# Kernel tuning notes

Hardware: AMD Instinct MI355X
Metric: run time of the kernel (lower is better)

Reference implementation:

```python
import jax, jax.numpy as jnp
import numpy as np

N = 100000
IN_DIM = 256
HID = 64
HEADS = 2
OUT_DIM = 64
E = 1600000
NEG_SLOPE = 0.2


def gat_conv(x, edge_index, W, att_src, att_dst, bias):
    # PyG GATConv with heads=HEADS, concat=True, add_self_loops=True.
    # x: [N, IN_DIM]; edge_index: [2, E] (row0=src, row1=dst)
    loops = jnp.arange(N, dtype=edge_index.dtype)
    src = jnp.concatenate([edge_index[0], loops])  # [E+N]
    dst = jnp.concatenate([edge_index[1], loops])  # [E+N]
    h = (x @ W).reshape(N, HEADS, HID)             # [N, H, C]
    a_src = jnp.einsum('nhc,hc->nh', h, att_src)   # [N, H]
    a_dst = jnp.einsum('nhc,hc->nh', h, att_dst)   # [N, H]
    e = jax.nn.leaky_relu(a_src[src] + a_dst[dst], NEG_SLOPE)  # [E+N, H]
    # segment softmax over incoming edges of each dst node
    m = jax.ops.segment_max(e, dst, num_segments=N)            # [N, H]
    p = jnp.exp(e - m[dst])
    denom = jax.ops.segment_sum(p, dst, num_segments=N)        # [N, H]
    alpha = p / denom[dst]                                     # [E+N, H]
    msg = h[src] * alpha[:, :, None]                           # [E+N, H, C]
    out = jax.ops.segment_sum(msg, dst, num_segments=N)        # [N, H, C]
    return out.reshape(N, HEADS * HID) + bias


def setup_inputs() -> dict:
    key = jax.random.key(0)
    ks = jax.random.split(key, 12)
    s_in = 1.0 / np.sqrt(IN_DIM)
    s_h = 1.0 / np.sqrt(HID)
    s_fc = 1.0 / np.sqrt(HEADS * HID * 2)
    return {
        'x': jax.random.normal(ks[0], (N, IN_DIM), jnp.float32),
        'edge_index_connected': jax.random.randint(ks[1], (2, E), 0, N, jnp.int32),
        'edge_index_liked': jax.random.randint(ks[2], (2, E), 0, N, jnp.int32),
        'W1': jax.random.normal(ks[3], (IN_DIM, HEADS * HID), jnp.float32) * s_in,
        'att_src1': jax.random.normal(ks[4], (HEADS, HID), jnp.float32) * s_h,
        'att_dst1': jax.random.normal(ks[5], (HEADS, HID), jnp.float32) * s_h,
        'b1': jnp.zeros((HEADS * HID,), jnp.float32),
        'W2': jax.random.normal(ks[6], (IN_DIM, HEADS * HID), jnp.float32) * s_in,
        'att_src2': jax.random.normal(ks[7], (HEADS, HID), jnp.float32) * s_h,
        'att_dst2': jax.random.normal(ks[8], (HEADS, HID), jnp.float32) * s_h,
        'b2': jnp.zeros((HEADS * HID,), jnp.float32),
        'fc_W': jax.random.normal(ks[9], (HEADS * HID * 2, OUT_DIM), jnp.float32) * s_fc,
        'fc_b': jnp.zeros((OUT_DIM,), jnp.float32),
    }


def reference(x, edge_index_connected, edge_index_liked, W1, att_src1, att_dst1, b1,
              W2, att_src2, att_dst2, b2, fc_W, fc_b):
    xc = jax.nn.relu(gat_conv(x, edge_index_connected, W1, att_src1, att_dst1, b1))
    xl = jax.nn.relu(gat_conv(x, edge_index_liked, W2, att_src2, att_dst2, b2))
    x_comb = jnp.concatenate([xc, xl], axis=1)  # [N, 4*HID]
    return x_comb @ fc_W + fc_b
```

## Files before the change

### kernel.cpp

```cpp
#include <hip/hip_runtime.h>
#include <hip/hip_fp16.h>
#include <math.h>

#define NN 100000
#define IN_DIM 256
#define HCH 128
#define OUT_DIM 64
#define EE 1600000
#define NEG_SLOPE 0.2f

#define NB 1024
#define NPB 98
#define CAP 2048

#define GEMM_BLOCKS 1563
#define CONV_BLOCKS 320
#define BUCKET_PER_LAYER 512
#define SORT_BLOCKS (2 * NB)

typedef _Float16 half8v __attribute__((ext_vector_type(8)));
typedef _Float16 half4v __attribute__((ext_vector_type(4)));
typedef __fp16 fp16x2 __attribute__((ext_vector_type(2)));
typedef float float4v __attribute__((ext_vector_type(4)));
typedef unsigned int u32;

union H2U { u32 u; fp16x2 h; };

__device__ __forceinline__ float lrelu(float v) { return v > 0.f ? v : NEG_SLOPE * v; }

__global__ __launch_bounds__(256, 8) void prep_kernel(
    const float* __restrict__ W0, const float* __restrict__ W1,
    const float* __restrict__ fcW,
    _Float16* __restrict__ wt, _Float16* __restrict__ fcw2,
    const int* __restrict__ ei0, const int* __restrict__ ei1,
    int* __restrict__ gcursor, int* __restrict__ bstore)
{
    __shared__ int hist[NB];
    __shared__ int base[NB];
    const int tid = threadIdx.x;

    if (blockIdx.x < CONV_BLOCKS) {
        int i = blockIdx.x * 256 + tid;
        if (i < 2 * IN_DIM * HCH) {
            int l = i >> 15, rem = i & 32767;
            int c = rem >> 8, k = rem & 255;
            const float* W = l ? W1 : W0;
            wt[i] = (_Float16)W[(size_t)k * HCH + c];
            return;
        }
        int j = i - 2 * IN_DIM * HCH;
        if (j < 256 * OUT_DIM) {
            int c = j >> 8, k = j & 255;
            fcw2[j] = (_Float16)fcW[(size_t)k * OUT_DIM + c];
        }
        return;
    }

    const int bb = blockIdx.x - CONV_BLOCKS;
    const int lay = bb >> 9;
    const int idx = bb & 511;
    const int* src = lay ? ei1 : ei0;
    const int* dst = src + EE;
    int* gcur = gcursor + lay * NB;
    int* bst = bstore + (size_t)lay * NB * CAP;

    const int per = (EE + BUCKET_PER_LAYER - 1) / BUCKET_PER_LAYER;
    const int e0 = idx * per;
    const int e1 = min(EE, e0 + per);
    for (int i = tid; i < NB; i += 256) hist[i] = 0;
    __syncthreads();
    for (int i = e0 + tid; i < e1; i += 256)
        atomicAdd(&hist[dst[i] / NPB], 1);
    __syncthreads();
    for (int b = tid; b < NB; b += 256) {
        int c = hist[b];
        base[b] = c ? atomicAdd(&gcur[b], c) : 0;
        hist[b] = 0;
    }
    __syncthreads();
    for (int i = e0 + tid; i < e1; i += 256) {
        int d = dst[i];
        int s = src[i];
        int b = d / NPB;
        int pos = base[b] + atomicAdd(&hist[b], 1);
        if (pos >= 0 && pos < CAP) bst[b * CAP + pos] = (s << 7) | (d - b * NPB);
    }
}

__global__ __launch_bounds__(256, 3) void mid_kernel(
    const float* __restrict__ x, const _Float16* __restrict__ wt,
    const float* __restrict__ attS0, const float* __restrict__ attD0,
    const float* __restrict__ attS1, const float* __restrict__ attD1,
    _Float16* __restrict__ h16, float* __restrict__ a_s, float* __restrict__ a_d,
    const int* __restrict__ gcursor, int* __restrict__ bstore,
    int* __restrict__ gstart, int* __restrict__ gend, int n)
{
    __shared__ __align__(16) _Float16 smem[64 * 72 + 256 * 72];
    __shared__ float attv[4][128];
    const int tid = threadIdx.x;

    const long long TS = SORT_BLOCKS;
    const long long TB = GEMM_BLOCKS + SORT_BLOCKS;
    const int k = blockIdx.x;
    const int slo = (int)(((long long)k * TS) / TB);
    const int shi = (int)(((long long)(k + 1) * TS) / TB);

    if (shi > slo) {
        int* raw = (int*)smem;
        int* sorted = raw + CAP;
        int* curs = sorted + CAP;
        int* scanbuf = curs + 128;
        const int sb = slo;
        const int lay = sb >> 10;
        const int b = sb & (NB - 1);
        const int* gcur = gcursor + lay * NB;
        int* bst = bstore + (size_t)lay * NB * CAP;
        int* gs = gstart + (size_t)lay * NN;
        int* ge = gend + (size_t)lay * NN;

        const int node0 = b * NPB;
        const int nnode = min(NPB, n - node0);
        if (nnode <= 0) return;
        int cnt = gcur[b];
        cnt = cnt < 0 ? 0 : (cnt > CAP ? CAP : cnt);

        for (int i = tid; i < cnt; i += 256) raw[i] = bst[b * CAP + i];
        if (tid < 128) curs[tid] = 0;
        __syncthreads();
        for (int i = tid; i < cnt; i += 256) atomicAdd(&curs[raw[i] & 127], 1);
        __syncthreads();
        if (tid < 128) scanbuf[tid] = curs[tid];
        __syncthreads();
        for (int off = 1; off < 128; off <<= 1) {
            int v = 0;
            if (tid < 128) { v = scanbuf[tid]; if (tid >= off) v += scanbuf[tid - off]; }
            __syncthreads();
            if (tid < 128) scanbuf[tid] = v;
            __syncthreads();
        }
        if (tid < 128) {
            int ex = tid ? scanbuf[tid - 1] : 0;
            curs[tid] = ex;
            if (tid < nnode) {
                gs[node0 + tid] = b * CAP + ex;
                ge[node0 + tid] = b * CAP + scanbuf[tid];
            }
        }
        __syncthreads();
        for (int i = tid; i < cnt; i += 256) {
            int item = raw[i];
            int pos = atomicAdd(&curs[item & 127], 1);
            if (pos >= 0 && pos < CAP) sorted[pos] = item >> 7;
        }
        __syncthreads();
        for (int i = tid; i < cnt; i += 256) bst[b * CAP + i] = sorted[i];
        return;
    }

    _Float16 (*As)[72] = (_Float16(*)[72])smem;
    _Float16 (*Bs)[72] = (_Float16(*)[72])(smem + 64 * 72);
    const int gb = k - slo;
    const int lane = tid & 63, wave = tid >> 6;
    const int wm = wave & 1, wn = wave >> 1;
    const int q = lane >> 4, r16 = lane & 15;
    const int row0 = gb * 64;

    if (tid < 128) {
        attv[0][tid] = attS0[tid]; attv[1][tid] = attD0[tid];
        attv[2][tid] = attS1[tid]; attv[3][tid] = attD1[tid];
    }

    float4v acc[2][8];
#pragma unroll
    for (int i = 0; i < 2; ++i)
#pragma unroll
        for (int j = 0; j < 8; ++j) acc[i][j] = (float4v){0.f, 0.f, 0.f, 0.f};

    const int ar = tid >> 2, aq = tid & 3;
    const bool rok = (row0 + ar) < n;
    for (int kt = 0; kt < IN_DIM; kt += 64) {
        const float* xp = x + (size_t)(row0 + ar) * IN_DIM + kt + aq * 16;
#pragma unroll
        for (int i = 0; i < 4; ++i) {
            float4 v = rok ? *(const float4*)(xp + i * 4) : make_float4(0.f, 0.f, 0.f, 0.f);
            half4v hv = { (_Float16)v.x, (_Float16)v.y, (_Float16)v.z, (_Float16)v.w };
            *(half4v*)&As[ar][aq * 16 + i * 4] = hv;
        }
        const _Float16* wp = wt + (size_t)tid * IN_DIM + kt;
#pragma unroll
        for (int i = 0; i < 8; ++i)
            *(half8v*)&Bs[tid][i * 8] = *(const half8v*)(wp + i * 8);
        __syncthreads();
#pragma unroll
        for (int s = 0; s < 2; ++s) {
            half8v af[2], bf[8];
#pragma unroll
            for (int t = 0; t < 2; ++t)
                af[t] = *(half8v*)&As[wm * 32 + t * 16 + r16][s * 32 + q * 8];
#pragma unroll
            for (int t = 0; t < 8; ++t)
                bf[t] = *(half8v*)&Bs[wn * 128 + t * 16 + r16][s * 32 + q * 8];
#pragma unroll
            for (int mt = 0; mt < 2; ++mt)
#pragma unroll
                for (int nt = 0; nt < 8; ++nt)
                    acc[mt][nt] = __builtin_amdgcn_mfma_f32_16x16x32_f16(
                        af[mt], bf[nt], acc[mt][nt], 0, 0, 0);
        }
        __syncthreads();
    }
    _Float16 (*eb)[264] = (_Float16(*)[264])smem;
#pragma unroll
    for (int mt = 0; mt < 2; ++mt) {
        const int er = wm * 32 + mt * 16 + q * 4;
#pragma unroll
        for (int reg = 0; reg < 4; ++reg)
#pragma unroll
            for (int nt = 0; nt < 8; ++nt)
                eb[er + reg][wn * 128 + nt * 16 + r16] = (_Float16)acc[mt][nt][reg];
    }
    __syncthreads();
    const int r = tid >> 2, qq = tid & 3;
    const int grow = row0 + r;
    if (grow < n) {
        const int l2 = qq >> 1;
        const int hh = qq & 1;
        const float* avS = &attv[l2 * 2 + 0][hh * 64];
        const float* avD = &attv[l2 * 2 + 1][hh * 64];
        _Float16* hout = h16 + (size_t)l2 * NN * HCH + (size_t)grow * HCH + hh * 64;
        float ds = 0.f, dd = 0.f;
#pragma unroll
        for (int i = 0; i < 8; ++i) {
            half8v v = *(half8v*)&eb[r][qq * 64 + i * 8];
            *(half8v*)(hout + i * 8) = v;
#pragma unroll
            for (int j = 0; j < 8; ++j) {
                float f = (float)v[j];
                ds = fmaf(f, avS[i * 8 + j], ds);
                dd = fmaf(f, avD[i * 8 + j], dd);
            }
        }
        a_s[(size_t)l2 * 2 * NN + 2 * grow + hh] = ds;
        a_d[(size_t)l2 * 2 * NN + 2 * grow + hh] = dd;
    }
}

__global__ __launch_bounds__(256) void agg_kernel(
    const _Float16* __restrict__ h16, const float2* __restrict__ a_s,
    const float2* __restrict__ a_d, const int* __restrict__ gstart,
    const int* __restrict__ gend, const int* __restrict__ bstore,
    const float* __restrict__ bias0, const float* __restrict__ bias1,
    _Float16* __restrict__ xc16, int n)
{
    __shared__ __align__(16) uint2 sh[4][64];
    const int lay = blockIdx.y;
    const _Float16* hL = h16 + (size_t)lay * NN * HCH;
    const float2* asL = a_s + (size_t)lay * NN;
    const float2* adL = a_d + (size_t)lay * NN;
    const int* gsL = gstart + (size_t)lay * NN;
    const int* geL = gend + (size_t)lay * NN;
    const int* ssort = bstore + (size_t)lay * NB * CAP;
    const float* bias = lay ? bias1 : bias0;

    const int wid = threadIdx.x >> 6, lane = threadIdx.x & 63;
    const int g = lane >> 4;
    const int i = lane & 15;
    const int hh = i >> 3;
    const u32 psel = hh ? 0x07060302u : 0x05040100u;
    const fp16x2 one2 = { (__fp16)1.f, (__fp16)1.f };

    const int node = blockIdx.x * 16 + wid * 4 + g;
    const bool valid = node < n;
    const int nn = valid ? node : 0;

    float bv[8];
#pragma unroll
    for (int j = 0; j < 8; ++j) bv[j] = bias[i * 8 + j];

    int start = gsL[nn], end = geL[nn];
    start = start < 0 ? 0 : (start > NB * CAP ? NB * CAP : start);
    end = end < start ? start : (end > NB * CAP ? NB * CAP : end);
    const int cnt = end - start;
    const float2 ad = adL[nn];
    const float2 asn = asL[nn];

    float acc[8] = {0.f, 0.f, 0.f, 0.f, 0.f, 0.f, 0.f, 0.f};
    float den = 0.f;
    uint2* slots = &sh[wid][g * 16];

    for (int base = 0; base < cnt; base += 16) {
        const int idx = start + base + i;
        float p0 = 0.f, p1 = 0.f;
        int s = 0;
        if (idx < end) {
            s = ssort[idx];
            if ((unsigned)s >= (unsigned)n) s = 0;
            float2 a = asL[s];
            p0 = __expf(lrelu(a.x + ad.x));
            p1 = __expf(lrelu(a.y + ad.y));
        }
        H2U pk; pk.h = __builtin_amdgcn_cvt_pkrtz(p0, p1);
        slots[i] = make_uint2((u32)s, pk.u);
        __builtin_amdgcn_wave_barrier();
        const int c2 = min(16, cnt - base);
        for (int t = 0; t < c2; t += 2) {
            const uint4 rec = *(const uint4*)&slots[t];
            H2U pph; pph.u = __builtin_amdgcn_perm(rec.w, rec.y, psel);
            const half8v hv0 = *(const half8v*)(hL + ((rec.x << 7) | (u32)(i << 3)));
            const half8v hv1 = *(const half8v*)(hL + ((rec.z << 7) | (u32)(i << 3)));
            const u32* ap = (const u32*)&hv0;
            const u32* bp = (const u32*)&hv1;
#pragma unroll
            for (int d2 = 0; d2 < 4; ++d2) {
                H2U pe, po;
                pe.u = __builtin_amdgcn_perm(bp[d2], ap[d2], 0x05040100u);
                po.u = __builtin_amdgcn_perm(bp[d2], ap[d2], 0x07060302u);
                acc[2 * d2]     = __builtin_amdgcn_fdot2(pe.h, pph.h, acc[2 * d2], false);
                acc[2 * d2 + 1] = __builtin_amdgcn_fdot2(po.h, pph.h, acc[2 * d2 + 1], false);
            }
            den = __builtin_amdgcn_fdot2(pph.h, one2, den, false);
        }
        __builtin_amdgcn_wave_barrier();
    }
    {
        const float ps0 = __expf(lrelu(asn.x + ad.x));
        const float ps1 = __expf(lrelu(asn.y + ad.y));
        const half8v hv = *(const half8v*)(hL + (((u32)nn << 7) | (u32)(i << 3)));
        const float pl = hh ? ps1 : ps0;
#pragma unroll
        for (int j2 = 0; j2 < 8; ++j2)
            acc[j2] = fmaf(pl, (float)hv[j2], acc[j2]);
        den += pl;
    }
    if (valid) {
        const float inv = 1.f / den;
        half8v o;
#pragma unroll
        for (int j2 = 0; j2 < 8; ++j2)
            o[j2] = (_Float16)fmaxf(acc[j2] * inv + bv[j2], 0.f);
        *(half8v*)(xc16 + (size_t)node * 256 + lay * HCH + i * 8) = o;
    }
}

__global__ __launch_bounds__(256) void fc_mfma(const _Float16* __restrict__ xc16,
                                               const _Float16* __restrict__ fw2,
                                               const float* __restrict__ fcb,
                                               float* __restrict__ out, int n)
{
    __shared__ _Float16 axs[64][264];
    const int tid = threadIdx.x;
    const int lane = tid & 63, wave = tid >> 6;
    const int q = lane >> 4, r16 = lane & 15;
    const int row0 = blockIdx.x * 64;

#pragma unroll
    for (int i = 0; i < 8; ++i) {
        const int idx = i * 256 + tid;
        const int row = idx >> 5;
        const int kg = (idx & 31) * 8;
        half8v v = { 0, 0, 0, 0, 0, 0, 0, 0 };
        if (row0 + row < n)
            v = *(const half8v*)(xc16 + (size_t)(row0 + row) * 256 + kg);
        *(half8v*)&axs[row][kg] = v;
    }
    __syncthreads();

    float4v acc[4];
#pragma unroll
    for (int i = 0; i < 4; ++i) acc[i] = (float4v){0.f, 0.f, 0.f, 0.f};
#pragma unroll
    for (int s = 0; s < 8; ++s) {
        const half8v af = *(half8v*)&axs[wave * 16 + r16][s * 32 + q * 8];
#pragma unroll
        for (int nt = 0; nt < 4; ++nt) {
            const half8v bf =
                *(const half8v*)(fw2 + (size_t)(nt * 16 + r16) * 256 + s * 32 + q * 8);
            acc[nt] = __builtin_amdgcn_mfma_f32_16x16x32_f16(af, bf, acc[nt], 0, 0, 0);
        }
    }
#pragma unroll
    for (int nt = 0; nt < 4; ++nt) {
        const int col = nt * 16 + r16;
#pragma unroll
        for (int reg = 0; reg < 4; ++reg) {
            const int row = row0 + wave * 16 + q * 4 + reg;
            if (row < n)
                out[(size_t)row * OUT_DIM + col] = acc[nt][reg] + fcb[col];
        }
    }
}

extern "C" void kernel_launch(void* const* d_in, const int* in_sizes, int n_in,
                              void* d_out, int out_size, void* d_ws, size_t ws_size,
                              hipStream_t stream)
{
    const float* x = (const float*)d_in[0];
    const int* ei[2] = { (const int*)d_in[1], (const int*)d_in[2] };
    const float* W[2] = { (const float*)d_in[3], (const float*)d_in[7] };
    const float* attS[2] = { (const float*)d_in[4], (const float*)d_in[8] };
    const float* attD[2] = { (const float*)d_in[5], (const float*)d_in[9] };
    const float* bias[2] = { (const float*)d_in[6], (const float*)d_in[10] };
    const float* fcW = (const float*)d_in[11];
    const float* fcb = (const float*)d_in[12];
    float* out = (float*)d_out;

    char* p = (char*)d_ws;
    size_t need = 0;
    auto carve = [&](size_t bytes) {
        char* r = p;
        size_t b = (bytes + 255) & ~(size_t)255;
        p += b;
        need += b;
        return r;
    };
    _Float16* h16 = (_Float16*)carve((size_t)2 * NN * HCH * 2);
    _Float16* xc16 = (_Float16*)carve((size_t)NN * 256 * 2);
    _Float16* wt = (_Float16*)carve((size_t)2 * IN_DIM * HCH * 2);
    _Float16* fcw2 = (_Float16*)carve((size_t)256 * OUT_DIM * 2);
    float* a_s = (float*)carve((size_t)2 * NN * 8);
    float* a_d = (float*)carve((size_t)2 * NN * 8);
    int* gcursor = (int*)carve((size_t)2 * NB * 4);
    int* bstore = (int*)carve((size_t)2 * NB * CAP * 4);
    int* gstart = (int*)carve((size_t)2 * NN * 4);
    int* gend = (int*)carve((size_t)2 * NN * 4);
    if (need > ws_size) return;

    (void)hipMemsetAsync(gcursor, 0, (size_t)2 * NB * 4, stream);

    prep_kernel<<<CONV_BLOCKS + 2 * BUCKET_PER_LAYER, 256, 0, stream>>>(
        W[0], W[1], fcW, wt, fcw2, ei[0], ei[1], gcursor, bstore);

    mid_kernel<<<GEMM_BLOCKS + SORT_BLOCKS, 256, 0, stream>>>(
        x, wt, attS[0], attD[0], attS[1], attD[1],
        h16, a_s, a_d, gcursor, bstore, gstart, gend, NN);

    agg_kernel<<<dim3((NN + 15) / 16, 2), 256, 0, stream>>>(
        h16, (const float2*)a_s, (const float2*)a_d,
        gstart, gend, bstore, bias[0], bias[1], xc16, NN);

    fc_mfma<<<GEMM_BLOCKS, 256, 0, stream>>>(xc16, fcw2, fcb, out, NN);
}
```

Before: 468.6 us.

## Co-schedule edge bucketing with GEMM and split per-bucket sort into own kernel

Edge bucketing moves out of the prep kernel and is interleaved with the x@W GEMM blocks in one launch. The per-bucket sort becomes a separate kernel, and the memset is folded into the weight-conversion kernel. The GEMM K-tile drops from 64 to 32 so shared memory shrinks and occupancy can rise to 4 blocks per CU. The agg grid is flattened to 1D. The aim is to overlap the atomic-heavy bucketing with the compute-bound GEMM, at the cost of one extra launch and more GEMM k-loop barriers.

```diff
diff --git a/kernel.cpp b/kernel.cpp
--- a/kernel.cpp
+++ b/kernel.cpp
@@ -16,7 +16,9 @@
 #define GEMM_BLOCKS 1563
 #define CONV_BLOCKS 320
 #define BUCKET_PER_LAYER 512
-#define SORT_BLOCKS (2 * NB)
+#define BUCKET_BLOCKS (2 * BUCKET_PER_LAYER)
+#define WORK_BLOCKS (GEMM_BLOCKS + BUCKET_BLOCKS)
+#define AGG_X ((NN + 15) / 16)
 
 typedef _Float16 half8v __attribute__((ext_vector_type(8)));
 typedef _Float16 half4v __attribute__((ext_vector_type(4)));
@@ -28,137 +30,87 @@
 
 __device__ __forceinline__ float lrelu(float v) { return v > 0.f ? v : NEG_SLOPE * v; }
 
-__global__ __launch_bounds__(256, 8) void prep_kernel(
+__global__ __launch_bounds__(256) void conv_kernel(
     const float* __restrict__ W0, const float* __restrict__ W1,
     const float* __restrict__ fcW,
     _Float16* __restrict__ wt, _Float16* __restrict__ fcw2,
-    const int* __restrict__ ei0, const int* __restrict__ ei1,
-    int* __restrict__ gcursor, int* __restrict__ bstore)
-{
-    __shared__ int hist[NB];
-    __shared__ int base[NB];
+    int* __restrict__ gcursor)
+{
     const int tid = threadIdx.x;
-
-    if (blockIdx.x < CONV_BLOCKS) {
-        int i = blockIdx.x * 256 + tid;
-        if (i < 2 * IN_DIM * HCH) {
-            int l = i >> 15, rem = i & 32767;
-            int c = rem >> 8, k = rem & 255;
-            const float* W = l ? W1 : W0;
-            wt[i] = (_Float16)W[(size_t)k * HCH + c];
-            return;
-        }
-        int j = i - 2 * IN_DIM * HCH;
-        if (j < 256 * OUT_DIM) {
-            int c = j >> 8, k = j & 255;
-            fcw2[j] = (_Float16)fcW[(size_t)k * OUT_DIM + c];
-        }
+    if (blockIdx.x == CONV_BLOCKS) {
+        for (int i = tid; i < 2 * NB; i += 256) gcursor[i] = 0;
         return;
     }
-
-    const int bb = blockIdx.x - CONV_BLOCKS;
-    const int lay = bb >> 9;
-    const int idx = bb & 511;
-    const int* src = lay ? ei1 : ei0;
-    const int* dst = src + EE;
-    int* gcur = gcursor + lay * NB;
-    int* bst = bstore + (size_t)lay * NB * CAP;
-
-    const int per = (EE + BUCKET_PER_LAYER - 1) / BUCKET_PER_LAYER;
-    const int e0 = idx * per;
-    const int e1 = min(EE, e0 + per);
-    for (int i = tid; i < NB; i += 256) hist[i] = 0;
-    __syncthreads();
-    for (int i = e0 + tid; i < e1; i += 256)
-        atomicAdd(&hist[dst[i] / NPB], 1);
-    __syncthreads();
-    for (int b = tid; b < NB; b += 256) {
-        int c = hist[b];
-        base[b] = c ? atomicAdd(&gcur[b], c) : 0;
-        hist[b] = 0;
-    }
-    __syncthreads();
-    for (int i = e0 + tid; i < e1; i += 256) {
-        int d = dst[i];
-        int s = src[i];
-        int b = d / NPB;
-        int pos = base[b] + atomicAdd(&hist[b], 1);
-        if (pos >= 0 && pos < CAP) bst[b * CAP + pos] = (s << 7) | (d - b * NPB);
-    }
-}
-
-__global__ __launch_bounds__(256, 3) void mid_kernel(
+    int i = blockIdx.x * 256 + tid;
+    if (i < 2 * IN_DIM * HCH) {
+        int l = i >> 15, rem = i & 32767;
+        int c = rem >> 8, k = rem & 255;
+        const float* W = l ? W1 : W0;
+        wt[i] = (_Float16)W[(size_t)k * HCH + c];
+        return;
+    }
+    int j = i - 2 * IN_DIM * HCH;
+    if (j < 256 * OUT_DIM) {
+        int c = j >> 8, k = j & 255;
+        fcw2[j] = (_Float16)fcW[(size_t)k * OUT_DIM + c];
+    }
+}
+
+__global__ __launch_bounds__(256, 4) void work_kernel(
     const float* __restrict__ x, const _Float16* __restrict__ wt,
     const float* __restrict__ attS0, const float* __restrict__ attD0,
     const float* __restrict__ attS1, const float* __restrict__ attD1,
     _Float16* __restrict__ h16, float* __restrict__ a_s, float* __restrict__ a_d,
-    const int* __restrict__ gcursor, int* __restrict__ bstore,
-    int* __restrict__ gstart, int* __restrict__ gend, int n)
-{
-    __shared__ __align__(16) _Float16 smem[64 * 72 + 256 * 72];
+    const int* __restrict__ ei0, const int* __restrict__ ei1,
+    int* __restrict__ gcursor, int* __restrict__ bstore, int n)
+{
+    __shared__ __align__(16) _Float16 smem[64 * 264];
     __shared__ float attv[4][128];
     const int tid = threadIdx.x;
 
-    const long long TS = SORT_BLOCKS;
-    const long long TB = GEMM_BLOCKS + SORT_BLOCKS;
+    const long long TS = BUCKET_BLOCKS;
+    const long long TB = WORK_BLOCKS;
     const int k = blockIdx.x;
     const int slo = (int)(((long long)k * TS) / TB);
     const int shi = (int)(((long long)(k + 1) * TS) / TB);
 
     if (shi > slo) {
-        int* raw = (int*)smem;
-        int* sorted = raw + CAP;
-        int* curs = sorted + CAP;
-        int* scanbuf = curs + 128;
-        const int sb = slo;
-        const int lay = sb >> 10;
-        const int b = sb & (NB - 1);
-        const int* gcur = gcursor + lay * NB;
+        int* hist = (int*)smem;
+        int* base = hist + NB;
+        const int bb = slo;
+        const int lay = bb >> 9;
+        const int idx = bb & 511;
+        const int* src = lay ? ei1 : ei0;
+        const int* dst = src + EE;
+        int* gcur = gcursor + lay * NB;
         int* bst = bstore + (size_t)lay * NB * CAP;
-        int* gs = gstart + (size_t)lay * NN;
-        int* ge = gend + (size_t)lay * NN;
-
-        const int node0 = b * NPB;
-        const int nnode = min(NPB, n - node0);
-        if (nnode <= 0) return;
-        int cnt = gcur[b];
-        cnt = cnt < 0 ? 0 : (cnt > CAP ? CAP : cnt);
-
-        for (int i = tid; i < cnt; i += 256) raw[i] = bst[b * CAP + i];
-        if (tid < 128) curs[tid] = 0;
-        __syncthreads();
-        for (int i = tid; i < cnt; i += 256) atomicAdd(&curs[raw[i] & 127], 1);
-        __syncthreads();
-        if (tid < 128) scanbuf[tid] = curs[tid];
-        __syncthreads();
-        for (int off = 1; off < 128; off <<= 1) {
-            int v = 0;
-            if (tid < 128) { v = scanbuf[tid]; if (tid >= off) v += scanbuf[tid - off]; }
-            __syncthreads();
-            if (tid < 128) scanbuf[tid] = v;
-            __syncthreads();
-        }
-        if (tid < 128) {
-            int ex = tid ? scanbuf[tid - 1] : 0;
-            curs[tid] = ex;
-            if (tid < nnode) {
-                gs[node0 + tid] = b * CAP + ex;
-                ge[node0 + tid] = b * CAP + scanbuf[tid];
-            }
-        }
-        __syncthreads();
-        for (int i = tid; i < cnt; i += 256) {
-            int item = raw[i];
-            int pos = atomicAdd(&curs[item & 127], 1);
-            if (pos >= 0 && pos < CAP) sorted[pos] = item >> 7;
-        }
-        __syncthreads();
-        for (int i = tid; i < cnt; i += 256) bst[b * CAP + i] = sorted[i];
+
+        const int per = (EE + BUCKET_PER_LAYER - 1) / BUCKET_PER_LAYER;
+        const int e0 = idx * per;
+        const int e1 = min(EE, e0 + per);
+        for (int i = tid; i < NB; i += 256) hist[i] = 0;
+        __syncthreads();
+        for (int i = e0 + tid; i < e1; i += 256)
+            atomicAdd(&hist[dst[i] / NPB], 1);
+        __syncthreads();
+        for (int b = tid; b < NB; b += 256) {
+            int c = hist[b];
+            base[b] = c ? atomicAdd(&gcur[b], c) : 0;
+            hist[b] = 0;
+        }
+        __syncthreads();
+        for (int i = e0 + tid; i < e1; i += 256) {
+            int d = dst[i];
+            int s = src[i];
+            int b = d / NPB;
+            int pos = base[b] + atomicAdd(&hist[b], 1);
+            if (pos >= 0 && pos < CAP) bst[b * CAP + pos] = (s << 7) | (d - b * NPB);
+        }
         return;
     }
 
-    _Float16 (*As)[72] = (_Float16(*)[72])smem;
-    _Float16 (*Bs)[72] = (_Float16(*)[72])(smem + 64 * 72);
+    _Float16 (*As)[40] = (_Float16(*)[40])smem;
+    _Float16 (*Bs)[40] = (_Float16(*)[40])(smem + 64 * 40);
     const int gb = k - slo;
     const int lane = tid & 63, wave = tid >> 6;
     const int wm = wave & 1, wn = wave >> 1;
@@ -178,34 +130,34 @@
 
     const int ar = tid >> 2, aq = tid & 3;
     const bool rok = (row0 + ar) < n;
-    for (int kt = 0; kt < IN_DIM; kt += 64) {
-        const float* xp = x + (size_t)(row0 + ar) * IN_DIM + kt + aq * 16;
-#pragma unroll
-        for (int i = 0; i < 4; ++i) {
-            float4 v = rok ? *(const float4*)(xp + i * 4) : make_float4(0.f, 0.f, 0.f, 0.f);
-            half4v hv = { (_Float16)v.x, (_Float16)v.y, (_Float16)v.z, (_Float16)v.w };
-            *(half4v*)&As[ar][aq * 16 + i * 4] = hv;
-        }
+    for (int kt = 0; kt < IN_DIM; kt += 32) {
+        const float* xp = x + (size_t)(row0 + ar) * IN_DIM + kt + aq * 8;
+        float4 v0 = rok ? *(const float4*)xp : make_float4(0.f, 0.f, 0.f, 0.f);
+        float4 v1 = rok ? *(const float4*)(xp + 4) : make_float4(0.f, 0.f, 0.f, 0.f);
+        half8v hv = { (_Float16)v0.x, (_Float16)v0.y, (_Float16)v0.z, (_Float16)v0.w,
+                      (_Float16)v1.x, (_Float16)v1.y, (_Float16)v1.z, (_Float16)v1.w };
+        *(half8v*)&As[ar][aq * 8] = hv;
         const _Float16* wp = wt + (size_t)tid * IN_DIM + kt;
 #pragma unroll
-        for (int i = 0; i < 8; ++i)
+        for (int i = 0; i < 4; ++i)
             *(half8v*)&Bs[tid][i * 8] = *(const half8v*)(wp + i * 8);
         __syncthreads();
-#pragma unroll
-        for (int s = 0; s < 2; ++s) {
-            half8v af[2], bf[8];
-#pragma unroll
-            for (int t = 0; t < 2; ++t)
-                af[t] = *(half8v*)&As[wm * 32 + t * 16 + r16][s * 32 + q * 8];
-#pragma unroll
-            for (int t = 0; t < 8; ++t)
-                bf[t] = *(half8v*)&Bs[wn * 128 + t * 16 + r16][s * 32 + q * 8];
+        half8v af[2];
+#pragma unroll
+        for (int t = 0; t < 2; ++t)
+            af[t] = *(half8v*)&As[wm * 32 + t * 16 + r16][q * 8];
+#pragma unroll
+        for (int hf = 0; hf < 2; ++hf) {
+            half8v bf[4];
+#pragma unroll
+            for (int j = 0; j < 4; ++j)
+                bf[j] = *(half8v*)&Bs[wn * 128 + (hf * 4 + j) * 16 + r16][q * 8];
 #pragma unroll
             for (int mt = 0; mt < 2; ++mt)
 #pragma unroll
-                for (int nt = 0; nt < 8; ++nt)
-                    acc[mt][nt] = __builtin_amdgcn_mfma_f32_16x16x32_f16(
-                        af[mt], bf[nt], acc[mt][nt], 0, 0, 0);
+                for (int j = 0; j < 4; ++j)
+                    acc[mt][hf * 4 + j] = __builtin_amdgcn_mfma_f32_16x16x32_f16(
+                        af[mt], bf[j], acc[mt][hf * 4 + j], 0, 0, 0);
         }
         __syncthreads();
     }
@@ -245,6 +197,60 @@
     }
 }
 
+__global__ __launch_bounds__(256) void sort_kernel(
+    const int* __restrict__ gcursor, int* __restrict__ bstore,
+    int* __restrict__ gstart, int* __restrict__ gend, int n)
+{
+    __shared__ int raw[CAP];
+    __shared__ int sorted[CAP];
+    __shared__ int curs[128];
+    __shared__ int scanbuf[128];
+    const int lay = blockIdx.y;
+    const int* gcur = gcursor + lay * NB;
+    int* bst = bstore + (size_t)lay * NB * CAP;
+    int* gs = gstart + (size_t)lay * NN;
+    int* ge = gend + (size_t)lay * NN;
+
+    const int tid = threadIdx.x;
+    const int b = blockIdx.x;
+    const int node0 = b * NPB;
+    const int nnode = min(NPB, n - node0);
+    if (nnode <= 0) return;
+    int cnt = gcur[b];
+    cnt = cnt < 0 ? 0 : (cnt > CAP ? CAP : cnt);
+
+    for (int i = tid; i < cnt; i += 256) raw[i] = bst[b * CAP + i];
+    if (tid < 128) curs[tid] = 0;
+    __syncthreads();
+    for (int i = tid; i < cnt; i += 256) atomicAdd(&curs[raw[i] & 127], 1);
+    __syncthreads();
+    if (tid < 128) scanbuf[tid] = curs[tid];
+    __syncthreads();
+    for (int off = 1; off < 128; off <<= 1) {
+        int v = 0;
+        if (tid < 128) { v = scanbuf[tid]; if (tid >= off) v += scanbuf[tid - off]; }
+        __syncthreads();
+        if (tid < 128) scanbuf[tid] = v;
+        __syncthreads();
+    }
+    if (tid < 128) {
+        int ex = tid ? scanbuf[tid - 1] : 0;
+        curs[tid] = ex;
+        if (tid < nnode) {
+            gs[node0 + tid] = b * CAP + ex;
+            ge[node0 + tid] = b * CAP + scanbuf[tid];
+        }
+    }
+    __syncthreads();
+    for (int i = tid; i < cnt; i += 256) {
+        int item = raw[i];
+        int pos = atomicAdd(&curs[item & 127], 1);
+        if (pos >= 0 && pos < CAP) sorted[pos] = item >> 7;
+    }
+    __syncthreads();
+    for (int i = tid; i < cnt; i += 256) bst[b * CAP + i] = sorted[i];
+}
+
 __global__ __launch_bounds__(256) void agg_kernel(
     const _Float16* __restrict__ h16, const float2* __restrict__ a_s,
     const float2* __restrict__ a_d, const int* __restrict__ gstart,
@@ -253,7 +259,9 @@
     _Float16* __restrict__ xc16, int n)
 {
     __shared__ __align__(16) uint2 sh[4][64];
-    const int lay = blockIdx.y;
+    int bx = blockIdx.x;
+    const int lay = bx >= AGG_X;
+    bx -= lay ? AGG_X : 0;
     const _Float16* hL = h16 + (size_t)lay * NN * HCH;
     const float2* asL = a_s + (size_t)lay * NN;
     const float2* adL = a_d + (size_t)lay * NN;
@@ -269,7 +277,7 @@
     const u32 psel = hh ? 0x07060302u : 0x05040100u;
     const fp16x2 one2 = { (__fp16)1.f, (__fp16)1.f };
 
-    const int node = blockIdx.x * 16 + wid * 4 + g;
+    const int node = bx * 16 + wid * 4 + g;
     const bool valid = node < n;
     const int nn = valid ? node : 0;
 
@@ -425,16 +433,15 @@
     int* gend = (int*)carve((size_t)2 * NN * 4);
     if (need > ws_size) return;
 
-    (void)hipMemsetAsync(gcursor, 0, (size_t)2 * NB * 4, stream);
-
-    prep_kernel<<<CONV_BLOCKS + 2 * BUCKET_PER_LAYER, 256, 0, stream>>>(
-        W[0], W[1], fcW, wt, fcw2, ei[0], ei[1], gcursor, bstore);
-
-    mid_kernel<<<GEMM_BLOCKS + SORT_BLOCKS, 256, 0, stream>>>(
+    conv_kernel<<<CONV_BLOCKS + 1, 256, 0, stream>>>(W[0], W[1], fcW, wt, fcw2, gcursor);
+
+    work_kernel<<<WORK_BLOCKS, 256, 0, stream>>>(
         x, wt, attS[0], attD[0], attS[1], attD[1],
-        h16, a_s, a_d, gcursor, bstore, gstart, gend, NN);
-
-    agg_kernel<<<dim3((NN + 15) / 16, 2), 256, 0, stream>>>(
+        h16, a_s, a_d, ei[0], ei[1], gcursor, bstore, NN);
+
+    sort_kernel<<<dim3(NB, 2), 256, 0, stream>>>(gcursor, bstore, gstart, gend, NN);
+
+    agg_kernel<<<2 * AGG_X, 256, 0, stream>>>(
         h16, (const float2*)a_s, (const float2*)a_d,
         gstart, gend, bstore, bias[0], bias[1], xc16, NN);
 
```

Result: faster. 458.0 us (-2.3%).
